# Optimization experiments

Measured on AMD Instinct MI355X. Metric: run time of the kernel, lower is better.

The kernel has to match this reference:

```python
import jax, jax.numpy as jnp
import numpy as np

N = 100000
E = 1600000
F_IN, HID, N_CLS = 128, 16, 32


def setup_inputs() -> dict:
    key = jax.random.key(0)
    ks = jax.random.split(key, 10)
    x = jax.random.normal(ks[0], (N, F_IN), dtype=jnp.float32)
    edge_index = jax.random.randint(ks[1], (2, E), 0, N, dtype=jnp.int64)
    edge_weight = jax.random.uniform(ks[2], (E,), dtype=jnp.float32)
    def glorot(k, shape):
        lim = np.sqrt(6.0 / (shape[0] + shape[1])).astype(np.float32)
        return jax.random.uniform(k, shape, dtype=jnp.float32, minval=-lim, maxval=lim)
    return {
        'x': x, 'edge_index': edge_index, 'edge_weight': edge_weight,
        'W1_0': glorot(ks[3], (F_IN, HID)), 'W1_1': glorot(ks[4], (F_IN, HID)),
        'b1': jnp.zeros((HID,), jnp.float32),
        'W2_0': glorot(ks[5], (HID, N_CLS)), 'W2_1': glorot(ks[6], (HID, N_CLS)),
        'b2': jnp.zeros((N_CLS,), jnp.float32),
    }


def _cheb_conv_k2(x, row, col, edge_weight, W0, W1, b):
    # PyG ChebConv, K=2, lambda_max=2.0:
    #   T0 = x; T1 = L_hat x = D^{-1/2} A D^{-1/2} x - x
    n = x.shape[0]
    deg = jax.ops.segment_sum(edge_weight, row, num_segments=n)  # [N]
    dinv = jnp.where(deg > 0, jax.lax.rsqrt(deg), 0.0)
    norm = dinv[row] * edge_weight * dinv[col]                   # [E]
    agg = jax.ops.segment_sum(norm[:, None] * x[col], row, num_segments=n)  # [N,F]
    tx1 = agg - x
    return x @ W0 + tx1 @ W1 + b


def reference(x, edge_index, edge_weight, W1_0, W1_1, b1, W2_0, W2_1, b2):
    row, col = edge_index[0], edge_index[1]
    h = jax.nn.relu(_cheb_conv_k2(x, row, col, edge_weight, W1_0, W1_1, b1))
    # dropout(p=0) and DFA layers are identity in forward
    out = _cheb_conv_k2(h, row, col, edge_weight, W2_0, W2_1, b2)
    return jax.nn.log_softmax(out, axis=1)
```

## Files before the change

kernel.cpp:

```cpp
#include <hip/hip_runtime.h>
#include <hip/hip_bf16.h>


#include <hip/hip_fp16.h>

constexpr int NN   = 100000;
constexpr int NE   = 1600000;
constexpr int FIN  = 128;
constexpr int HID  = 16;
constexpr int NCLS = 32;

constexpr int RB    = 256;
constexpr int NBKT  = (NN + RB - 1) / RB;
constexpr int EPB   = 4096;
constexpr int EPT   = EPB / 256;
constexpr int GP    = (NE + EPB - 1) / EPB;
constexpr int CAP   = 8192;
constexpr int NTILE = NN / 16;
constexpr int NPAIR = NN / 2;

typedef float f32x2 __attribute__((ext_vector_type(2)));
typedef float f32x4 __attribute__((ext_vector_type(4)));
typedef short bf16x8 __attribute__((ext_vector_type(8)));

#if defined(__has_builtin)
#if __has_builtin(__builtin_amdgcn_cvt_pk_f32_fp8)
#define HAVE_CVT_FP8 1
#endif
#endif

static __device__ __forceinline__ unsigned int f2e4m3(float f) {
    union { float f; unsigned int u; } v; v.f = f;
    unsigned int s = (v.u >> 24) & 0x80u;
    unsigned int au = v.u & 0x7fffffffu;
    if (au > 0x43E00000u) au = 0x43E00000u;
    au += 0x7ffffu + ((au >> 20) & 1u);
    int e4 = (int)(au >> 23) - 120;
    unsigned int m = (au >> 20) & 7u;
    unsigned int byte = (e4 <= 0) ? 0u : (((unsigned int)e4 << 3) | m);
    return s | byte;
}
static __device__ __forceinline__ void fp8x4_fma(unsigned int v, float w, float* acc) {
#ifdef HAVE_CVT_FP8
    f32x2 lo = __builtin_amdgcn_cvt_pk_f32_fp8((int)v, false);
    f32x2 hi = __builtin_amdgcn_cvt_pk_f32_fp8((int)v, true);
    acc[0] += w * lo.x; acc[1] += w * lo.y;
    acc[2] += w * hi.x; acc[3] += w * hi.y;
#else
#pragma unroll
    for (int i = 0; i < 4; i++) {
        unsigned int b = (v >> (8 * i)) & 0xffu;
        float f = __int_as_float((int)(((b & 0x80u) << 24) | ((b & 0x7fu) << 20))) * 0x1p120f;
        acc[i] += w * f;
    }
#endif
}
static __device__ __forceinline__ unsigned short f2bf(float f) {
    union { float f; unsigned int u; } v; v.f = f;
    unsigned int r = v.u + 0x7fffu + ((v.u >> 16) & 1u);
    return (unsigned short)(r >> 16);
}
static __device__ __forceinline__ float bf2f(unsigned short b) {
    union { unsigned int u; float f; } v; v.u = ((unsigned int)b) << 16;
    return v.f;
}
static __device__ __forceinline__ unsigned int wpack(float wf) {
    unsigned int b = __float_as_uint(wf) + 0x8000u;
    return (b >> 16) & 0x7fffu;
}
static __device__ __forceinline__ float wdec(unsigned int u) {
    return __uint_as_float((u >> 17) << 16);
}

__global__ void k_zero_cur(int* __restrict__ bucketCursor) {
    int i = blockIdx.x * blockDim.x + threadIdx.x;
    if (i < NBKT) bucketCursor[i] = 0;
}

__global__ __launch_bounds__(256) void k_partition(
    const int* __restrict__ row, const int* __restrict__ col,
    const float* __restrict__ w, int* __restrict__ bucketCursor,
    int2* __restrict__ partS) {
    __shared__ int2 stage[EPB];
    __shared__ unsigned short sbkt[EPB];
    __shared__ int cnt[NBKT];
    __shared__ int lofs[NBKT];
    __shared__ int cursor[NBKT];
    __shared__ int gbase[NBKT];
    __shared__ int sa[512], sb[512];
    int tid = threadIdx.x;
    long ebase = (long)blockIdx.x * EPB;
    int rr[EPT]; int cc[EPT]; float wv[EPT];
#pragma unroll
    for (int i = 0; i < EPT; i++) {
        long e = ebase + i * 256 + tid;
        if (e < NE) { rr[i] = row[e]; cc[i] = col[e]; wv[i] = w[e]; }
        else rr[i] = -1;
    }
    for (int i = tid; i < NBKT; i += 256) cnt[i] = 0;
    __syncthreads();
#pragma unroll
    for (int i = 0; i < EPT; i++)
        if (rr[i] >= 0) atomicAdd(&cnt[rr[i] >> 8], 1);
    __syncthreads();
    for (int i = tid; i < 512; i += 256) sa[i] = (i < NBKT) ? cnt[i] : 0;
    __syncthreads();
    int* src = sa; int* dst = sb;
    for (int off = 1; off < 512; off <<= 1) {
        for (int i = tid; i < 512; i += 256)
            dst[i] = src[i] + ((i >= off) ? src[i - off] : 0);
        __syncthreads();
        int* t = src; src = dst; dst = t;
    }
    for (int i = tid; i < NBKT; i += 256) {
        int ex = src[i] - cnt[i];
        lofs[i] = ex;
        cursor[i] = ex;
        int go = (cnt[i] > 0) ? atomicAdd(&bucketCursor[i], cnt[i]) : 0;
        gbase[i] = i * CAP + go;
    }
    __syncthreads();
#pragma unroll
    for (int i = 0; i < EPT; i++) {
        if (rr[i] >= 0) {
            int b = rr[i] >> 8;
            int p = atomicAdd(&cursor[b], 1);
            int2 v;
            v.x = cc[i] | ((rr[i] & 255) << 17);
            v.y = __float_as_int(wv[i]);
            stage[p] = v;
            sbkt[p] = (unsigned short)b;
        }
    }
    __syncthreads();
    int total = (int)min((long)EPB, NE - ebase);
    for (int i = tid; i < total; i += 256) {
        int b = sbkt[i];
        partS[gbase[b] + (i - lofs[b])] = stage[i];
    }
}

__global__ __launch_bounds__(256) void k_bucket_sort(
    const int2* __restrict__ partS, const int* __restrict__ bucketCursor,
    unsigned int* __restrict__ partC, int* __restrict__ rowptr,
    float* __restrict__ dinv) {
    __shared__ int hist[RB];
    __shared__ int cursor[RB];
    __shared__ float dsum[RB];
    __shared__ int wtot[4];
    __shared__ int red[4];
    int b = blockIdx.x;
    int tid = threadIdx.x;
    int lane = tid & 63, wv = tid >> 6;
    int partial = 0;
    for (int i = tid; i < b; i += 256) partial += bucketCursor[i];
#pragma unroll
    for (int off = 1; off < 64; off <<= 1) partial += __shfl_xor(partial, off, 64);
    if (lane == 0) red[wv] = partial;
    hist[tid] = 0;
    dsum[tid] = 0.f;
    __syncthreads();
    int start = red[0] + red[1] + red[2] + red[3];
    int count = bucketCursor[b];
    const int2* src = partS + (long)b * CAP;
    for (int i = tid; i < count; i += 256)
        atomicAdd(&hist[((unsigned)src[i].x >> 17) & 255], 1);
    __syncthreads();
    int v = hist[tid];
    int sc = v;
#pragma unroll
    for (int off = 1; off < 64; off <<= 1) {
        int up = __shfl_up(sc, off, 64);
        if (lane >= off) sc += up;
    }
    if (lane == 63) wtot[wv] = sc;
    __syncthreads();
    int add = 0;
    for (int w2 = 0; w2 < wv; w2++) add += wtot[w2];
    int ex = sc + add - v;
    int node = b * RB + tid;
    if (node <= NN) rowptr[node] = start + ex;
    cursor[tid] = ex;
    __syncthreads();
    for (int i = tid; i < count; i += 256) {
        int2 p = src[i];
        int rl = ((unsigned)p.x >> 17) & 255;
        int pos = atomicAdd(&cursor[rl], 1);
        float wf = __int_as_float(p.y);
        partC[start + pos] = ((unsigned)p.x & 0x1FFFFu) | (wpack(wf) << 17);
        atomicAdd(&dsum[rl], wf);
    }
    __syncthreads();
    if (node < NN) {
        float dsv = dsum[tid];
        dinv[node] = dsv > 0.f ? rsqrtf(dsv) : 0.f;
    }
}

__global__ __launch_bounds__(256) void k_proj1(
    const float* __restrict__ x, const float* __restrict__ W0,
    const float* __restrict__ W1, const float* __restrict__ b1,
    const float* __restrict__ dinv,
    float* __restrict__ xa, unsigned char* __restrict__ xb8) {
    int wid = (int)(((long)blockIdx.x * 256 + threadIdx.x) >> 6);
    if (wid >= NTILE) return;
    int lane = threadIdx.x & 63;
    int col = lane & 15, quad = lane >> 4;

    bf16x8 bfrag[2][4];
#pragma unroll
    for (int mat = 0; mat < 2; mat++) {
        const float* W = mat ? W1 : W0;
#pragma unroll
        for (int kb = 0; kb < 4; kb++) {
            bf16x8 f;
#pragma unroll
            for (int j = 0; j < 8; j++)
                f[j] = (short)f2bf(W[(kb * 32 + quad * 8 + j) * HID + col]);
            bfrag[mat][kb] = f;
        }
    }

    const float* xrow = x + ((long)wid * 16 + col) * FIN + quad * 8;
    float4 xb[8];
#pragma unroll
    for (int kb = 0; kb < 4; kb++) {
        xb[2 * kb]     = *(const float4*)(xrow + kb * 32);
        xb[2 * kb + 1] = *(const float4*)(xrow + kb * 32 + 4);
    }
    f32x4 acc0 = {0.f, 0.f, 0.f, 0.f}, acc1 = {0.f, 0.f, 0.f, 0.f};
#pragma unroll
    for (int kb = 0; kb < 4; kb++) {
        float4 a0 = xb[2 * kb], a1 = xb[2 * kb + 1];
        bf16x8 af;
        af[0] = (short)f2bf(a0.x); af[1] = (short)f2bf(a0.y);
        af[2] = (short)f2bf(a0.z); af[3] = (short)f2bf(a0.w);
        af[4] = (short)f2bf(a1.x); af[5] = (short)f2bf(a1.y);
        af[6] = (short)f2bf(a1.z); af[7] = (short)f2bf(a1.w);
        acc0 = __builtin_amdgcn_mfma_f32_16x16x32_bf16(af, bfrag[0][kb], acc0, 0, 0, 0);
        acc1 = __builtin_amdgcn_mfma_f32_16x16x32_bf16(af, bfrag[1][kb], acc1, 0, 0, 0);
    }

    float b1v = b1[col];
#pragma unroll
    for (int r = 0; r < 4; r++) {
        long node = (long)wid * 16 + quad * 4 + r;
        float a0 = acc0[r], a1 = acc1[r];
        xa[node * HID + col] = a0 - a1 + b1v;
        float dn = dinv[node];
        xb8[node * HID + col] = (unsigned char)f2e4m3(dn * a1);
    }
}

__global__ __launch_bounds__(256) void k_gather1(
    const int* __restrict__ rowptr, const unsigned int* __restrict__ partC,
    const float* __restrict__ dinv, const unsigned char* __restrict__ xb8,
    const float* __restrict__ xa,
    unsigned short* __restrict__ h16, unsigned char* __restrict__ h8) {
    long t = (long)blockIdx.x * 256 + threadIdx.x;
    int w = (int)(t >> 6);
    if (w >= NPAIR) return;
    int lane = threadIdx.x & 63;
    int d = lane & 3, p = lane >> 2;
    long n0 = (long)w * 2, n1 = n0 + 1;

    int s0 = rowptr[n0], e0 = rowptr[n0 + 1], e1 = rowptr[n0 + 2];
    float2 dnv = *(const float2*)(dinv + n0);
    float4 xav0 = *(const float4*)(xa + n0 * HID + d * 4);
    float4 xav1 = *(const float4*)(xa + n1 * HID + d * 4);

    float acc0[4] = {0.f, 0.f, 0.f, 0.f};
    float acc1[4] = {0.f, 0.f, 0.f, 0.f};
    int j0 = s0 + p, j1 = e0 + p;
    while ((j0 < e0) | (j1 < e1)) {
        if (j0 < e0) {
            unsigned int u = partC[j0];
            unsigned int v = *(const unsigned int*)(xb8 + (u & 0x1FFFF) * HID + d * 4);
            fp8x4_fma(v, wdec(u), acc0);
            j0 += 16;
        }
        if (j1 < e1) {
            unsigned int u = partC[j1];
            unsigned int v = *(const unsigned int*)(xb8 + (u & 0x1FFFF) * HID + d * 4);
            fp8x4_fma(v, wdec(u), acc1);
            j1 += 16;
        }
    }
#pragma unroll
    for (int i = 0; i < 4; i++) {
        acc0[i] += __shfl_xor(acc0[i], 4);  acc1[i] += __shfl_xor(acc1[i], 4);
        acc0[i] += __shfl_xor(acc0[i], 8);  acc1[i] += __shfl_xor(acc1[i], 8);
        acc0[i] += __shfl_xor(acc0[i], 16); acc1[i] += __shfl_xor(acc1[i], 16);
        acc0[i] += __shfl_xor(acc0[i], 32); acc1[i] += __shfl_xor(acc1[i], 32);
    }
    if (p == 0) {
        float h0[4], h1[4];
        h0[0] = fmaxf(xav0.x + dnv.x * acc0[0], 0.f);
        h0[1] = fmaxf(xav0.y + dnv.x * acc0[1], 0.f);
        h0[2] = fmaxf(xav0.z + dnv.x * acc0[2], 0.f);
        h0[3] = fmaxf(xav0.w + dnv.x * acc0[3], 0.f);
        h1[0] = fmaxf(xav1.x + dnv.y * acc1[0], 0.f);
        h1[1] = fmaxf(xav1.y + dnv.y * acc1[1], 0.f);
        h1[2] = fmaxf(xav1.z + dnv.y * acc1[2], 0.f);
        h1[3] = fmaxf(xav1.w + dnv.y * acc1[3], 0.f);
        ushort4 u0, u1;
        u0.x = f2bf(h0[0]); u0.y = f2bf(h0[1]); u0.z = f2bf(h0[2]); u0.w = f2bf(h0[3]);
        u1.x = f2bf(h1[0]); u1.y = f2bf(h1[1]); u1.z = f2bf(h1[2]); u1.w = f2bf(h1[3]);
        *(ushort4*)(h16 + n0 * HID + d * 4) = u0;
        *(ushort4*)(h16 + n1 * HID + d * 4) = u1;
        unsigned int p0 = f2e4m3(dnv.x * h0[0]) | (f2e4m3(dnv.x * h0[1]) << 8)
                        | (f2e4m3(dnv.x * h0[2]) << 16) | (f2e4m3(dnv.x * h0[3]) << 24);
        unsigned int p1 = f2e4m3(dnv.y * h1[0]) | (f2e4m3(dnv.y * h1[1]) << 8)
                        | (f2e4m3(dnv.y * h1[2]) << 16) | (f2e4m3(dnv.y * h1[3]) << 24);
        *(unsigned int*)(h8 + n0 * HID + d * 4) = p0;
        *(unsigned int*)(h8 + n1 * HID + d * 4) = p1;
    }
}

__global__ __launch_bounds__(256) void k_gather2(
    const int* __restrict__ rowptr, const unsigned int* __restrict__ partC,
    const float* __restrict__ dinv, const unsigned char* __restrict__ h8,
    unsigned short* __restrict__ g16) {
    long t = (long)blockIdx.x * 256 + threadIdx.x;
    int w = (int)(t >> 6);
    if (w >= NPAIR) return;
    int lane = threadIdx.x & 63;
    int d = lane & 3, p = lane >> 2;
    long n0 = (long)w * 2, n1 = n0 + 1;

    int s0 = rowptr[n0], e0 = rowptr[n0 + 1], e1 = rowptr[n0 + 2];
    float2 dnv = *(const float2*)(dinv + n0);

    float acc0[4] = {0.f, 0.f, 0.f, 0.f};
    float acc1[4] = {0.f, 0.f, 0.f, 0.f};
    int j0 = s0 + p, j1 = e0 + p;
    while ((j0 < e0) | (j1 < e1)) {
        if (j0 < e0) {
            unsigned int u = partC[j0];
            unsigned int v = *(const unsigned int*)(h8 + (u & 0x1FFFF) * HID + d * 4);
            fp8x4_fma(v, wdec(u), acc0);
            j0 += 16;
        }
        if (j1 < e1) {
            unsigned int u = partC[j1];
            unsigned int v = *(const unsigned int*)(h8 + (u & 0x1FFFF) * HID + d * 4);
            fp8x4_fma(v, wdec(u), acc1);
            j1 += 16;
        }
    }
#pragma unroll
    for (int i = 0; i < 4; i++) {
        acc0[i] += __shfl_xor(acc0[i], 4);  acc1[i] += __shfl_xor(acc1[i], 4);
        acc0[i] += __shfl_xor(acc0[i], 8);  acc1[i] += __shfl_xor(acc1[i], 8);
        acc0[i] += __shfl_xor(acc0[i], 16); acc1[i] += __shfl_xor(acc1[i], 16);
        acc0[i] += __shfl_xor(acc0[i], 32); acc1[i] += __shfl_xor(acc1[i], 32);
    }
    if (p == 0) {
        ushort4 u0, u1;
        u0.x = f2bf(dnv.x * acc0[0]); u0.y = f2bf(dnv.x * acc0[1]);
        u0.z = f2bf(dnv.x * acc0[2]); u0.w = f2bf(dnv.x * acc0[3]);
        u1.x = f2bf(dnv.y * acc1[0]); u1.y = f2bf(dnv.y * acc1[1]);
        u1.z = f2bf(dnv.y * acc1[2]); u1.w = f2bf(dnv.y * acc1[3]);
        *(ushort4*)(g16 + n0 * HID + d * 4) = u0;
        *(ushort4*)(g16 + n1 * HID + d * 4) = u1;
    }
}

__global__ __launch_bounds__(256) void k_lsm(
    const unsigned short* __restrict__ h16, const unsigned short* __restrict__ g16,
    const float* __restrict__ W0, const float* __restrict__ W1,
    const float* __restrict__ b2, float* __restrict__ out) {
    int wid = (int)(((long)blockIdx.x * 256 + threadIdx.x) >> 6);
    if (wid >= NTILE) return;
    int lane = threadIdx.x & 63;
    int col = lane & 15, quad = lane >> 4;

    bf16x8 bfrag[2];
#pragma unroll
    for (int c = 0; c < 2; c++) {
        bf16x8 f;
        if (quad < 2) {
#pragma unroll
            for (int j = 0; j < 8; j++) {
                int k = quad * 8 + j;
                f[j] = (short)f2bf(W0[k * NCLS + col + 16 * c] - W1[k * NCLS + col + 16 * c]);
            }
        } else {
#pragma unroll
            for (int j = 0; j < 8; j++) {
                int k = (quad - 2) * 8 + j;
                f[j] = (short)f2bf(W1[k * NCLS + col + 16 * c]);
            }
        }
        bfrag[c] = f;
    }

    long node_a = (long)wid * 16 + col;
    const unsigned short* abase =
        (quad & 2) ? (g16 + node_a * HID + (quad & 1) * 8)
                   : (h16 + node_a * HID + (quad & 1) * 8);
    bf16x8 af = *(const bf16x8*)abase;

    f32x4 c0 = {0.f, 0.f, 0.f, 0.f}, c1 = {0.f, 0.f, 0.f, 0.f};
    c0 = __builtin_amdgcn_mfma_f32_16x16x32_bf16(af, bfrag[0], c0, 0, 0, 0);
    c1 = __builtin_amdgcn_mfma_f32_16x16x32_bf16(af, bfrag[1], c1, 0, 0, 0);

    float b2a = b2[col], b2b = b2[col + 16];
#pragma unroll
    for (int r = 0; r < 4; r++) {
        long node = (long)wid * 16 + quad * 4 + r;
        float v0 = c0[r] + b2a;
        float v1 = c1[r] + b2b;
        float m = fmaxf(v0, v1);
        m = fmaxf(m, __shfl_xor(m, 1));
        m = fmaxf(m, __shfl_xor(m, 2));
        m = fmaxf(m, __shfl_xor(m, 4));
        m = fmaxf(m, __shfl_xor(m, 8));
        float sum = __expf(v0 - m) + __expf(v1 - m);
        sum += __shfl_xor(sum, 1);
        sum += __shfl_xor(sum, 2);
        sum += __shfl_xor(sum, 4);
        sum += __shfl_xor(sum, 8);
        float ls = logf(sum);
        out[node * NCLS + col] = v0 - m - ls;
        out[node * NCLS + col + 16] = v1 - m - ls;
    }
}

extern "C" void kernel_launch(void* const* d_in, const int* in_sizes, int n_in,
                              void* d_out, int out_size, void* d_ws, size_t ws_size,
                              hipStream_t stream) {
    const float* x    = (const float*)d_in[0];
    const int*   ei   = (const int*)d_in[1];
    const float* ew   = (const float*)d_in[2];
    const float* W1_0 = (const float*)d_in[3];
    const float* W1_1 = (const float*)d_in[4];
    const float* b1   = (const float*)d_in[5];
    const float* W2_0 = (const float*)d_in[6];
    const float* W2_1 = (const float*)d_in[7];
    const float* b2   = (const float*)d_in[8];
    float* out = (float*)d_out;

    const int* row = ei;
    const int* col = ei + NE;

    char* ws = (char*)d_ws;
    int2*  partS     = (int2*)ws;                 ws += sizeof(int2) * (long)NBKT * CAP;
    unsigned int* partC = (unsigned int*)ws;      ws += sizeof(int) * NE;
    int*   bucketCursor = (int*)ws;               ws += sizeof(int) * NBKT;
    int*   rowptr    = (int*)ws;                  ws += sizeof(int) * (NN + 4);
    float* dinv      = (float*)ws;                ws += sizeof(float) * NN;
    float* xa        = (float*)ws;                ws += sizeof(float) * NN * HID;
    unsigned short* h16 = (unsigned short*)ws;    ws += sizeof(short) * NN * HID;
    unsigned short* g16 = (unsigned short*)ws;    ws += sizeof(short) * NN * HID;
    unsigned char* xb8 = (unsigned char*)ws;      ws += sizeof(char) * NN * HID;
    unsigned char* h8  = (unsigned char*)ws;      ws += sizeof(char) * NN * HID;

    k_zero_cur<<<(NBKT + 255) / 256, 256, 0, stream>>>(bucketCursor);
    k_partition<<<GP, 256, 0, stream>>>(row, col, ew, bucketCursor, partS);
    k_bucket_sort<<<NBKT, 256, 0, stream>>>(partS, bucketCursor, partC, rowptr, dinv);
    k_proj1<<<(NTILE * 64 + 255) / 256, 256, 0, stream>>>(x, W1_0, W1_1, b1, dinv, xa, xb8);
    {
        long th = (long)NPAIR * 64;
        k_gather1<<<(int)((th + 255) / 256), 256, 0, stream>>>(
            rowptr, partC, dinv, xb8, xa, h16, h8);
        k_gather2<<<(int)((th + 255) / 256), 256, 0, stream>>>(
            rowptr, partC, dinv, h8, g16);
    }
    k_lsm<<<(NTILE * 64 + 255) / 256, 256, 0, stream>>>(h16, g16, W2_0, W2_1, b2, out);
}
```

Before: 213.8 us.

## Fuse projection into bucket sort and gather2 into log-softmax kernel

Merges the layer-1 projection into the per-bucket sort kernel, which now reads dinv from shared memory, and merges the second-layer gather with the final MFMA plus log-softmax. Each block gathers 16 nodes into a shared tile and one wave finishes them. This removes two launches and the g16 global round trip. In exchange, in the fused output kernel three of four waves sit idle during the MFMA phase, and the gather now runs four nodes per wave, which may shift load balance and register pressure.

```diff
diff --git a/kernel.cpp b/kernel.cpp
--- a/kernel.cpp
+++ b/kernel.cpp
@@ -1,8 +1,7 @@
 #include <hip/hip_runtime.h>
 #include <hip/hip_bf16.h>
-
-
 #include <hip/hip_fp16.h>
+
 
 constexpr int NN   = 100000;
 constexpr int NE   = 1600000;
@@ -59,10 +58,6 @@
     union { float f; unsigned int u; } v; v.f = f;
     unsigned int r = v.u + 0x7fffu + ((v.u >> 16) & 1u);
     return (unsigned short)(r >> 16);
-}
-static __device__ __forceinline__ float bf2f(unsigned short b) {
-    union { unsigned int u; float f; } v; v.u = ((unsigned int)b) << 16;
-    return v.f;
 }
 static __device__ __forceinline__ unsigned int wpack(float wf) {
     unsigned int b = __float_as_uint(wf) + 0x8000u;
@@ -140,13 +135,17 @@
     }
 }
 
-__global__ __launch_bounds__(256) void k_bucket_sort(
+__global__ __launch_bounds__(256) void k_bucket_sort_proj1(
     const int2* __restrict__ partS, const int* __restrict__ bucketCursor,
     unsigned int* __restrict__ partC, int* __restrict__ rowptr,
-    float* __restrict__ dinv) {
+    float* __restrict__ dinv,
+    const float* __restrict__ x, const float* __restrict__ W1_0,
+    const float* __restrict__ W1_1, const float* __restrict__ b1,
+    float* __restrict__ xa, unsigned char* __restrict__ xb8) {
     __shared__ int hist[RB];
     __shared__ int cursor[RB];
     __shared__ float dsum[RB];
+    __shared__ float sh_dinv[RB];
     __shared__ int wtot[4];
     __shared__ int red[4];
     int b = blockIdx.x;
@@ -191,64 +190,64 @@
         atomicAdd(&dsum[rl], wf);
     }
     __syncthreads();
-    if (node < NN) {
+    {
         float dsv = dsum[tid];
-        dinv[node] = dsv > 0.f ? rsqrtf(dsv) : 0.f;
-    }
-}
-
-__global__ __launch_bounds__(256) void k_proj1(
-    const float* __restrict__ x, const float* __restrict__ W0,
-    const float* __restrict__ W1, const float* __restrict__ b1,
-    const float* __restrict__ dinv,
-    float* __restrict__ xa, unsigned char* __restrict__ xb8) {
-    int wid = (int)(((long)blockIdx.x * 256 + threadIdx.x) >> 6);
-    if (wid >= NTILE) return;
-    int lane = threadIdx.x & 63;
-    int col = lane & 15, quad = lane >> 4;
-
-    bf16x8 bfrag[2][4];
-#pragma unroll
-    for (int mat = 0; mat < 2; mat++) {
-        const float* W = mat ? W1 : W0;
-#pragma unroll
-        for (int kb = 0; kb < 4; kb++) {
-            bf16x8 f;
-#pragma unroll
-            for (int j = 0; j < 8; j++)
-                f[j] = (short)f2bf(W[(kb * 32 + quad * 8 + j) * HID + col]);
-            bfrag[mat][kb] = f;
-        }
-    }
-
-    const float* xrow = x + ((long)wid * 16 + col) * FIN + quad * 8;
-    float4 xb[8];
-#pragma unroll
-    for (int kb = 0; kb < 4; kb++) {
-        xb[2 * kb]     = *(const float4*)(xrow + kb * 32);
-        xb[2 * kb + 1] = *(const float4*)(xrow + kb * 32 + 4);
-    }
-    f32x4 acc0 = {0.f, 0.f, 0.f, 0.f}, acc1 = {0.f, 0.f, 0.f, 0.f};
-#pragma unroll
-    for (int kb = 0; kb < 4; kb++) {
-        float4 a0 = xb[2 * kb], a1 = xb[2 * kb + 1];
-        bf16x8 af;
-        af[0] = (short)f2bf(a0.x); af[1] = (short)f2bf(a0.y);
-        af[2] = (short)f2bf(a0.z); af[3] = (short)f2bf(a0.w);
-        af[4] = (short)f2bf(a1.x); af[5] = (short)f2bf(a1.y);
-        af[6] = (short)f2bf(a1.z); af[7] = (short)f2bf(a1.w);
-        acc0 = __builtin_amdgcn_mfma_f32_16x16x32_bf16(af, bfrag[0][kb], acc0, 0, 0, 0);
-        acc1 = __builtin_amdgcn_mfma_f32_16x16x32_bf16(af, bfrag[1][kb], acc1, 0, 0, 0);
-    }
-
-    float b1v = b1[col];
-#pragma unroll
-    for (int r = 0; r < 4; r++) {
-        long node = (long)wid * 16 + quad * 4 + r;
-        float a0 = acc0[r], a1 = acc1[r];
-        xa[node * HID + col] = a0 - a1 + b1v;
-        float dn = dinv[node];
-        xb8[node * HID + col] = (unsigned char)f2e4m3(dn * a1);
+        float dv = dsv > 0.f ? rsqrtf(dsv) : 0.f;
+        if (node < NN) dinv[node] = dv;
+        sh_dinv[tid] = dv;
+    }
+    __syncthreads();
+
+    {
+        int pcol = lane & 15, quad = lane >> 4;
+        bf16x8 bfrag[2][4];
+#pragma unroll
+        for (int mat = 0; mat < 2; mat++) {
+            const float* W = mat ? W1_1 : W1_0;
+#pragma unroll
+            for (int kb = 0; kb < 4; kb++) {
+                bf16x8 f;
+#pragma unroll
+                for (int j = 0; j < 8; j++)
+                    f[j] = (short)f2bf(W[(kb * 32 + quad * 8 + j) * HID + pcol]);
+                bfrag[mat][kb] = f;
+            }
+        }
+        float b1v = b1[pcol];
+#pragma unroll
+        for (int i = 0; i < 4; i++) {
+            int tb = wv * 4 + i;
+            int wid = b * 16 + tb;
+            if (wid >= NTILE) break;
+            const float* xrow = x + ((long)wid * 16 + pcol) * FIN + quad * 8;
+            float4 xb[8];
+#pragma unroll
+            for (int kb = 0; kb < 4; kb++) {
+                xb[2 * kb]     = *(const float4*)(xrow + kb * 32);
+                xb[2 * kb + 1] = *(const float4*)(xrow + kb * 32 + 4);
+            }
+            f32x4 acc0 = {0.f, 0.f, 0.f, 0.f}, acc1 = {0.f, 0.f, 0.f, 0.f};
+#pragma unroll
+            for (int kb = 0; kb < 4; kb++) {
+                float4 a0 = xb[2 * kb], a1 = xb[2 * kb + 1];
+                bf16x8 af;
+                af[0] = (short)f2bf(a0.x); af[1] = (short)f2bf(a0.y);
+                af[2] = (short)f2bf(a0.z); af[3] = (short)f2bf(a0.w);
+                af[4] = (short)f2bf(a1.x); af[5] = (short)f2bf(a1.y);
+                af[6] = (short)f2bf(a1.z); af[7] = (short)f2bf(a1.w);
+                acc0 = __builtin_amdgcn_mfma_f32_16x16x32_bf16(af, bfrag[0][kb], acc0, 0, 0, 0);
+                acc1 = __builtin_amdgcn_mfma_f32_16x16x32_bf16(af, bfrag[1][kb], acc1, 0, 0, 0);
+            }
+#pragma unroll
+            for (int r = 0; r < 4; r++) {
+                int lidx = tb * 16 + quad * 4 + r;
+                long nd = (long)b * RB + lidx;
+                float a0 = acc0[r], a1 = acc1[r];
+                xa[nd * HID + pcol] = a0 - a1 + b1v;
+                float dn = sh_dinv[lidx];
+                xb8[nd * HID + pcol] = (unsigned char)f2e4m3(dn * a1);
+            }
+        }
     }
 }
 
@@ -317,113 +316,132 @@
     }
 }
 
-__global__ __launch_bounds__(256) void k_gather2(
+__global__ __launch_bounds__(256) void k_gather2_lsm(
     const int* __restrict__ rowptr, const unsigned int* __restrict__ partC,
     const float* __restrict__ dinv, const unsigned char* __restrict__ h8,
-    unsigned short* __restrict__ g16) {
-    long t = (long)blockIdx.x * 256 + threadIdx.x;
-    int w = (int)(t >> 6);
-    if (w >= NPAIR) return;
-    int lane = threadIdx.x & 63;
+    const unsigned short* __restrict__ h16,
+    const float* __restrict__ W2_0, const float* __restrict__ W2_1,
+    const float* __restrict__ b2, float* __restrict__ out) {
+    __shared__ unsigned short sh_g[16][16];
+    int tile = blockIdx.x;
+    int tid = threadIdx.x;
+    int lane = tid & 63, wv = tid >> 6;
     int d = lane & 3, p = lane >> 2;
-    long n0 = (long)w * 2, n1 = n0 + 1;
-
-    int s0 = rowptr[n0], e0 = rowptr[n0 + 1], e1 = rowptr[n0 + 2];
-    float2 dnv = *(const float2*)(dinv + n0);
-
-    float acc0[4] = {0.f, 0.f, 0.f, 0.f};
-    float acc1[4] = {0.f, 0.f, 0.f, 0.f};
-    int j0 = s0 + p, j1 = e0 + p;
-    while ((j0 < e0) | (j1 < e1)) {
+    int nb = tile * 16 + wv * 4;
+
+    int s[5];
+#pragma unroll
+    for (int k = 0; k < 5; k++) s[k] = rowptr[nb + k];
+    float4 dn4 = *(const float4*)(dinv + nb);
+
+    float acc[4][4];
+#pragma unroll
+    for (int c = 0; c < 4; c++)
+#pragma unroll
+        for (int i = 0; i < 4; i++) acc[c][i] = 0.f;
+
+    int j0 = s[0] + p, j1 = s[1] + p, j2 = s[2] + p, j3 = s[3] + p;
+    int e0 = s[1], e1 = s[2], e2 = s[3], e3 = s[4];
+    while ((j0 < e0) | (j1 < e1) | (j2 < e2) | (j3 < e3)) {
         if (j0 < e0) {
             unsigned int u = partC[j0];
             unsigned int v = *(const unsigned int*)(h8 + (u & 0x1FFFF) * HID + d * 4);
-            fp8x4_fma(v, wdec(u), acc0);
+            fp8x4_fma(v, wdec(u), acc[0]);
             j0 += 16;
         }
         if (j1 < e1) {
             unsigned int u = partC[j1];
             unsigned int v = *(const unsigned int*)(h8 + (u & 0x1FFFF) * HID + d * 4);
-            fp8x4_fma(v, wdec(u), acc1);
+            fp8x4_fma(v, wdec(u), acc[1]);
             j1 += 16;
         }
+        if (j2 < e2) {
+            unsigned int u = partC[j2];
+            unsigned int v = *(const unsigned int*)(h8 + (u & 0x1FFFF) * HID + d * 4);
+            fp8x4_fma(v, wdec(u), acc[2]);
+            j2 += 16;
+        }
+        if (j3 < e3) {
+            unsigned int u = partC[j3];
+            unsigned int v = *(const unsigned int*)(h8 + (u & 0x1FFFF) * HID + d * 4);
+            fp8x4_fma(v, wdec(u), acc[3]);
+            j3 += 16;
+        }
     }
 #pragma unroll
     for (int i = 0; i < 4; i++) {
-        acc0[i] += __shfl_xor(acc0[i], 4);  acc1[i] += __shfl_xor(acc1[i], 4);
-        acc0[i] += __shfl_xor(acc0[i], 8);  acc1[i] += __shfl_xor(acc1[i], 8);
-        acc0[i] += __shfl_xor(acc0[i], 16); acc1[i] += __shfl_xor(acc1[i], 16);
-        acc0[i] += __shfl_xor(acc0[i], 32); acc1[i] += __shfl_xor(acc1[i], 32);
+        acc[0][i] += __shfl_xor(acc[0][i], 4);  acc[1][i] += __shfl_xor(acc[1][i], 4);
+        acc[2][i] += __shfl_xor(acc[2][i], 4);  acc[3][i] += __shfl_xor(acc[3][i], 4);
+        acc[0][i] += __shfl_xor(acc[0][i], 8);  acc[1][i] += __shfl_xor(acc[1][i], 8);
+        acc[2][i] += __shfl_xor(acc[2][i], 8);  acc[3][i] += __shfl_xor(acc[3][i], 8);
+        acc[0][i] += __shfl_xor(acc[0][i], 16); acc[1][i] += __shfl_xor(acc[1][i], 16);
+        acc[2][i] += __shfl_xor(acc[2][i], 16); acc[3][i] += __shfl_xor(acc[3][i], 16);
+        acc[0][i] += __shfl_xor(acc[0][i], 32); acc[1][i] += __shfl_xor(acc[1][i], 32);
+        acc[2][i] += __shfl_xor(acc[2][i], 32); acc[3][i] += __shfl_xor(acc[3][i], 32);
     }
     if (p == 0) {
-        ushort4 u0, u1;
-        u0.x = f2bf(dnv.x * acc0[0]); u0.y = f2bf(dnv.x * acc0[1]);
-        u0.z = f2bf(dnv.x * acc0[2]); u0.w = f2bf(dnv.x * acc0[3]);
-        u1.x = f2bf(dnv.y * acc1[0]); u1.y = f2bf(dnv.y * acc1[1]);
-        u1.z = f2bf(dnv.y * acc1[2]); u1.w = f2bf(dnv.y * acc1[3]);
-        *(ushort4*)(g16 + n0 * HID + d * 4) = u0;
-        *(ushort4*)(g16 + n1 * HID + d * 4) = u1;
-    }
-}
-
-__global__ __launch_bounds__(256) void k_lsm(
-    const unsigned short* __restrict__ h16, const unsigned short* __restrict__ g16,
-    const float* __restrict__ W0, const float* __restrict__ W1,
-    const float* __restrict__ b2, float* __restrict__ out) {
-    int wid = (int)(((long)blockIdx.x * 256 + threadIdx.x) >> 6);
-    if (wid >= NTILE) return;
-    int lane = threadIdx.x & 63;
-    int col = lane & 15, quad = lane >> 4;
-
-    bf16x8 bfrag[2];
-#pragma unroll
-    for (int c = 0; c < 2; c++) {
-        bf16x8 f;
-        if (quad < 2) {
-#pragma unroll
-            for (int j = 0; j < 8; j++) {
-                int k = quad * 8 + j;
-                f[j] = (short)f2bf(W0[k * NCLS + col + 16 * c] - W1[k * NCLS + col + 16 * c]);
+        float dnc[4] = {dn4.x, dn4.y, dn4.z, dn4.w};
+#pragma unroll
+        for (int c = 0; c < 4; c++) {
+            ushort4 u;
+            u.x = f2bf(dnc[c] * acc[c][0]); u.y = f2bf(dnc[c] * acc[c][1]);
+            u.z = f2bf(dnc[c] * acc[c][2]); u.w = f2bf(dnc[c] * acc[c][3]);
+            *(ushort4*)&sh_g[wv * 4 + c][d * 4] = u;
+        }
+    }
+    __syncthreads();
+
+    if (wv == 0) {
+        int pcol = lane & 15, quad = lane >> 4;
+        bf16x8 bfrag[2];
+#pragma unroll
+        for (int c = 0; c < 2; c++) {
+            bf16x8 f;
+            if (quad < 2) {
+#pragma unroll
+                for (int j = 0; j < 8; j++) {
+                    int k = quad * 8 + j;
+                    f[j] = (short)f2bf(W2_0[k * NCLS + pcol + 16 * c] - W2_1[k * NCLS + pcol + 16 * c]);
+                }
+            } else {
+#pragma unroll
+                for (int j = 0; j < 8; j++) {
+                    int k = (quad - 2) * 8 + j;
+                    f[j] = (short)f2bf(W2_1[k * NCLS + pcol + 16 * c]);
+                }
             }
-        } else {
-#pragma unroll
-            for (int j = 0; j < 8; j++) {
-                int k = (quad - 2) * 8 + j;
-                f[j] = (short)f2bf(W1[k * NCLS + col + 16 * c]);
-            }
-        }
-        bfrag[c] = f;
-    }
-
-    long node_a = (long)wid * 16 + col;
-    const unsigned short* abase =
-        (quad & 2) ? (g16 + node_a * HID + (quad & 1) * 8)
-                   : (h16 + node_a * HID + (quad & 1) * 8);
-    bf16x8 af = *(const bf16x8*)abase;
-
-    f32x4 c0 = {0.f, 0.f, 0.f, 0.f}, c1 = {0.f, 0.f, 0.f, 0.f};
-    c0 = __builtin_amdgcn_mfma_f32_16x16x32_bf16(af, bfrag[0], c0, 0, 0, 0);
-    c1 = __builtin_amdgcn_mfma_f32_16x16x32_bf16(af, bfrag[1], c1, 0, 0, 0);
-
-    float b2a = b2[col], b2b = b2[col + 16];
-#pragma unroll
-    for (int r = 0; r < 4; r++) {
-        long node = (long)wid * 16 + quad * 4 + r;
-        float v0 = c0[r] + b2a;
-        float v1 = c1[r] + b2b;
-        float m = fmaxf(v0, v1);
-        m = fmaxf(m, __shfl_xor(m, 1));
-        m = fmaxf(m, __shfl_xor(m, 2));
-        m = fmaxf(m, __shfl_xor(m, 4));
-        m = fmaxf(m, __shfl_xor(m, 8));
-        float sum = __expf(v0 - m) + __expf(v1 - m);
-        sum += __shfl_xor(sum, 1);
-        sum += __shfl_xor(sum, 2);
-        sum += __shfl_xor(sum, 4);
-        sum += __shfl_xor(sum, 8);
-        float ls = logf(sum);
-        out[node * NCLS + col] = v0 - m - ls;
-        out[node * NCLS + col + 16] = v1 - m - ls;
+            bfrag[c] = f;
+        }
+        bf16x8 af;
+        if (quad < 2)
+            af = *(const bf16x8*)(h16 + ((long)tile * 16 + pcol) * HID + (quad & 1) * 8);
+        else
+            af = *(const bf16x8*)&sh_g[pcol][(quad & 1) * 8];
+
+        f32x4 c0 = {0.f, 0.f, 0.f, 0.f}, c1 = {0.f, 0.f, 0.f, 0.f};
+        c0 = __builtin_amdgcn_mfma_f32_16x16x32_bf16(af, bfrag[0], c0, 0, 0, 0);
+        c1 = __builtin_amdgcn_mfma_f32_16x16x32_bf16(af, bfrag[1], c1, 0, 0, 0);
+
+        float b2a = b2[pcol], b2b = b2[pcol + 16];
+#pragma unroll
+        for (int r = 0; r < 4; r++) {
+            long node = (long)tile * 16 + quad * 4 + r;
+            float v0 = c0[r] + b2a;
+            float v1 = c1[r] + b2b;
+            float m = fmaxf(v0, v1);
+            m = fmaxf(m, __shfl_xor(m, 1));
+            m = fmaxf(m, __shfl_xor(m, 2));
+            m = fmaxf(m, __shfl_xor(m, 4));
+            m = fmaxf(m, __shfl_xor(m, 8));
+            float sum = __expf(v0 - m) + __expf(v1 - m);
+            sum += __shfl_xor(sum, 1);
+            sum += __shfl_xor(sum, 2);
+            sum += __shfl_xor(sum, 4);
+            sum += __shfl_xor(sum, 8);
+            float ls = logf(sum);
+            out[node * NCLS + pcol] = v0 - m - ls;
+            out[node * NCLS + pcol + 16] = v1 - m - ls;
+        }
     }
 }
 
@@ -452,20 +470,19 @@
     float* dinv      = (float*)ws;                ws += sizeof(float) * NN;
     float* xa        = (float*)ws;                ws += sizeof(float) * NN * HID;
     unsigned short* h16 = (unsigned short*)ws;    ws += sizeof(short) * NN * HID;
-    unsigned short* g16 = (unsigned short*)ws;    ws += sizeof(short) * NN * HID;
     unsigned char* xb8 = (unsigned char*)ws;      ws += sizeof(char) * NN * HID;
     unsigned char* h8  = (unsigned char*)ws;      ws += sizeof(char) * NN * HID;
 
     k_zero_cur<<<(NBKT + 255) / 256, 256, 0, stream>>>(bucketCursor);
     k_partition<<<GP, 256, 0, stream>>>(row, col, ew, bucketCursor, partS);
-    k_bucket_sort<<<NBKT, 256, 0, stream>>>(partS, bucketCursor, partC, rowptr, dinv);
-    k_proj1<<<(NTILE * 64 + 255) / 256, 256, 0, stream>>>(x, W1_0, W1_1, b1, dinv, xa, xb8);
+    k_bucket_sort_proj1<<<NBKT, 256, 0, stream>>>(partS, bucketCursor, partC,
+                                                  rowptr, dinv, x, W1_0, W1_1,
+                                                  b1, xa, xb8);
     {
         long th = (long)NPAIR * 64;
         k_gather1<<<(int)((th + 255) / 256), 256, 0, stream>>>(
             rowptr, partC, dinv, xb8, xa, h16, h8);
-        k_gather2<<<(int)((th + 255) / 256), 256, 0, stream>>>(
-            rowptr, partC, dinv, h8, g16);
-    }
-    k_lsm<<<(NTILE * 64 + 255) / 256, 256, 0, stream>>>(h16, g16, W2_0, W2_1, b2, out);
-}
+    }
+    k_gather2_lsm<<<NTILE, 256, 0, stream>>>(rowptr, partC, dinv, h8, h16,
+                                             W2_0, W2_1, b2, out);
+}
```

New measurement: 205.5 us. -3.9%, faster.
